# Optimization experiments

Hardware: AMD Instinct MI355X
Metric: run time of the kernel (lower is better)

The kernel has to match this reference:

```python
import jax, jax.numpy as jnp
import numpy as np

N_GRAPH = 10000
IN_DIM = 256
HID = 256
N_NODES = 16
FEAT_DIM = 64
N_EDGES = 5
TAU = 0.01


def _gat(x, src, dst, W, al, ar, R, b, H, D, N):
    # DGL GATConv: fc -> per-head attention logits -> edge softmax over dst -> aggregate, residual fc, bias
    h = (x @ W).reshape(N, H, D)                      # [N,H,D]
    el = jnp.sum(h * al[None], -1)                    # [N,H]
    er = jnp.sum(h * ar[None], -1)                    # [N,H]
    e = jax.nn.leaky_relu(el[src] + er[dst], 0.2)     # [E,H]
    m = jax.ops.segment_max(e, dst, num_segments=N)
    ex = jnp.exp(e - m[dst])
    s = jax.ops.segment_sum(ex, dst, num_segments=N)
    alpha = ex / s[dst]                               # [E,H]
    out = jax.ops.segment_sum(alpha[:, :, None] * h[src], dst, num_segments=N)  # [N,H,D]
    out = out + (x @ R).reshape(N, H, D) + b.reshape(1, H, D)
    return out.reshape(N, H * D)


def _masked_softmax(vec, mask, eps=1e-8):
    m = mask.astype(vec.dtype)
    _vec = vec * m - 10000.0 * (1.0 - m)
    vmax = jnp.max(_vec, axis=-1, keepdims=True)
    exps = jnp.exp((vec - vmax) * m) * m
    return exps / (jnp.sum(exps, -1, keepdims=True) + eps)


def _sample_edges(probs, target_idx):
    n, T = probs.shape
    mask = jnp.arange(T) == target_idx                # [T] bool, one-hot of target
    edges = [jnp.full((n,), target_idx, dtype=jnp.int32)]
    key = jax.random.key(42)
    for i in range(N_EDGES - 1):
        p = _masked_softmax(probs, jnp.logical_not(mask))
        idx = jax.random.categorical(jax.random.fold_in(key, i),
                                     jnp.log(jnp.maximum(p, 1e-30)), axis=-1)  # [n]
        mask = jnp.logical_or(jax.nn.one_hot(idx, T, dtype=bool), mask)
        edges.append(idx.astype(jnp.int32))
    return jnp.stack(edges, axis=-1)                  # [n, N_EDGES]


def _forward(feat, W1a, al1a, ar1a, R1a, b1a, W1e, al1e, ar1e, R1e, b1e,
             W2a, al2a, ar2a, R2a, b2a, W2e, al2e, ar2e, R2e, b2e,
             Wt, bt, Wo, bo, src, dst, target_idx):
    N = feat.shape[0]
    tf = jax.nn.leaky_relu(feat[target_idx] @ Wt + bt, 0.01)            # [2*HID]
    a = _gat(feat, src, dst, W1a, al1a, ar1a, R1a, b1a, 4, HID // 4, N)  # [N,HID]
    e = _gat(feat, src, dst, W1e, al1e, ar1e, R1e, b1e, 4, HID // 4, N)  # [N,HID]
    a2 = jax.nn.leaky_relu(jnp.concatenate([a, e], -1) + tf, 0.01)       # [N,2*HID]
    e2 = jax.nn.leaky_relu(jnp.concatenate([e, a], -1) + tf, 0.01)
    a3 = _gat(a2, src, dst, W2a, al2a, ar2a, R2a, b2a, 4, N_NODES * FEAT_DIM // 4, N)  # [N, n_nodes*feat_dim]
    e3 = _gat(e2, src, dst, W2e, al2e, ar2e, R2e, b2e, 1, N_NODES, N)                  # [N, n_nodes]
    attr = a3.reshape(N, N_NODES, FEAT_DIM).mean(0)                     # [n_nodes, feat_dim]
    node_attr = jax.nn.leaky_relu(attr, 0.01) @ Wo + bo                 # [n_nodes, input_dim]
    probs = jax.nn.softmax(e3.T, axis=-1)                               # [n_nodes, N]
    return node_attr, probs


def setup_inputs() -> dict:
    key = jax.random.key(0)
    ks = jax.random.split(key, 32)
    N, IN, H = N_GRAPH, IN_DIM, 4
    E0 = 80000
    feat = jax.random.normal(ks[0], (N, IN), jnp.float32)
    loop = jnp.arange(N, dtype=jnp.int32)
    src = jnp.concatenate([jax.random.randint(ks[1], (E0,), 0, N, jnp.int32), loop])
    dst = jnp.concatenate([jax.random.randint(ks[2], (E0,), 0, N, jnp.int32), loop])

    def p(k, shape, fan):
        return jax.random.normal(k, shape, jnp.float32) * (1.0 / np.sqrt(fan))

    D1 = HID // 4
    D2a = N_NODES * FEAT_DIM // 4
    O2a = N_NODES * FEAT_DIM
    inp = dict(feat=feat, src=src, dst=dst, target_idx=7)
    # layer-1 attr / edge GATs
    inp.update(W1a=p(ks[3], (IN, HID), IN), al1a=p(ks[4], (H, D1), D1), ar1a=p(ks[5], (H, D1), D1),
               R1a=p(ks[6], (IN, HID), IN), b1a=p(ks[7], (HID,), HID))
    inp.update(W1e=p(ks[8], (IN, HID), IN), al1e=p(ks[9], (H, D1), D1), ar1e=p(ks[10], (H, D1), D1),
               R1e=p(ks[11], (IN, HID), IN), b1e=p(ks[12], (HID,), HID))
    # layer-2 attr GAT (4 heads) and edge GAT (1 head)
    inp.update(W2a=p(ks[13], (2 * HID, O2a), 2 * HID), al2a=p(ks[14], (H, D2a), D2a), ar2a=p(ks[15], (H, D2a), D2a),
               R2a=p(ks[16], (2 * HID, O2a), 2 * HID), b2a=p(ks[17], (O2a,), O2a))
    inp.update(W2e=p(ks[18], (2 * HID, N_NODES), 2 * HID), al2e=p(ks[19], (1, N_NODES), N_NODES),
               ar2e=p(ks[20], (1, N_NODES), N_NODES), R2e=p(ks[21], (2 * HID, N_NODES), 2 * HID),
               b2e=p(ks[22], (N_NODES,), N_NODES))
    # target feat layer and attr output layer
    inp.update(Wt=p(ks[23], (IN, 2 * HID), IN), bt=p(ks[24], (2 * HID,), 2 * HID),
               Wo=p(ks[25], (FEAT_DIM, IN), FEAT_DIM), bo=p(ks[26], (IN,), IN))
    return inp


def reference(feat, W1a, al1a, ar1a, R1a, b1a, W1e, al1e, ar1e, R1e, b1e,
              W2a, al2a, ar2a, R2a, b2a, W2e, al2e, ar2e, R2e, b2e,
              Wt, bt, Wo, bo, src, dst, target_idx):
    node_attr, probs = _forward(feat, W1a, al1a, ar1a, R1a, b1a, W1e, al1e, ar1e, R1e, b1e,
                                W2a, al2a, ar2a, R2a, b2a, W2e, al2e, ar2e, R2e, b2e,
                                Wt, bt, Wo, bo, src, dst, target_idx)
    node_edges = _sample_edges(probs, target_idx)
    # (node_attr, attr_sample_weights, node_edges, normalized_edge_sample_weights)
    return node_attr, node_attr, node_edges, probs
```

## Files before the change

kernel.cpp:

```cpp
#include <hip/hip_runtime.h>
#include <hip/hip_bf16.h>

#define NGR 10000
typedef unsigned int u32;
typedef __attribute__((ext_vector_type(8))) short short8;
typedef __attribute__((ext_vector_type(4))) float f32x4;

__device__ __forceinline__ void threefry(u32 k0, u32 k1, u32 c0, u32 c1, u32& o0, u32& o1) {
    u32 ks2 = k0 ^ k1 ^ 0x1BD11BDAu;
    u32 x0 = c0 + k0, x1 = c1 + k1;
#define TF_R(r) { x0 += x1; x1 = (x1 << r) | (x1 >> (32 - r)); x1 ^= x0; }
    TF_R(13) TF_R(15) TF_R(26) TF_R(6)
    x0 += k1; x1 += ks2 + 1u;
    TF_R(17) TF_R(29) TF_R(16) TF_R(24)
    x0 += ks2; x1 += k0 + 2u;
    TF_R(13) TF_R(15) TF_R(26) TF_R(6)
    x0 += k0; x1 += k1 + 3u;
    TF_R(17) TF_R(29) TF_R(16) TF_R(24)
    x0 += k1; x1 += ks2 + 4u;
    TF_R(13) TF_R(15) TF_R(26) TF_R(6)
    x0 += ks2; x1 += k0 + 5u;
#undef TF_R
    o0 = x0; o1 = x1;
}

__global__ void k_deg(const int* __restrict__ dst, int* __restrict__ deg, int E) {
    int i = blockIdx.x * blockDim.x + threadIdx.x;
    if (i < E) atomicAdd(&deg[dst[i]], 1);
}
__global__ void k_scan(const int* __restrict__ deg, int* __restrict__ rowptr, int n) {
    __shared__ int sums[256];
    __shared__ int excl[257];
    const int T = 256;
    int t = threadIdx.x;
    int per = (n + T - 1) / T;
    int lo = t * per, hi = min(lo + per, n);
    int s = 0;
    for (int i = lo; i < hi; ++i) s += deg[i];
    sums[t] = s;
    __syncthreads();
    if (t == 0) { int run = 0; for (int i = 0; i < T; ++i) { excl[i] = run; run += sums[i]; } excl[T] = run; }
    __syncthreads();
    int run = excl[t];
    for (int i = lo; i < hi; ++i) { rowptr[i] = run; run += deg[i]; }
    if (t == 0) rowptr[n] = excl[T];
}
__global__ void k_scatter(const int* __restrict__ dst, const int* __restrict__ rowptr,
                          int* __restrict__ cursor, int* __restrict__ colidx, int E) {
    int i = blockIdx.x * blockDim.x + threadIdx.x;
    if (i >= E) return;
    int d = dst[i];
    int pos = atomicAdd(&cursor[d], 1);
    colidx[rowptr[d] + pos] = i;
}

#define TINYF 1.17549435e-38f
__global__ __launch_bounds__(256) void k_prep(
    const float* __restrict__ feat, const int* __restrict__ tptr,
    const float* __restrict__ Wt, const float* __restrict__ bt,
    const float* __restrict__ W1a, const float* __restrict__ W1e,
    const float* __restrict__ R1a, const float* __restrict__ R1e,
    const float* __restrict__ b1a, const float* __restrict__ b1e,
    const float* __restrict__ W2a, const float* __restrict__ al2a, const float* __restrict__ ar2a,
    unsigned short* __restrict__ feathi, unsigned short* __restrict__ featlo,
    unsigned short* __restrict__ WThi, unsigned short* __restrict__ WTlo,
    float* __restrict__ tf, float* __restrict__ gum, float* __restrict__ wal,
    float* __restrict__ packb, float* __restrict__ zreg)
{
    __shared__ float sh[32 * 33];
    int b = blockIdx.x, tid = threadIdx.x;
    if (b < 2500) {
        int idx = b * 256 + tid;
        float4 v = ((const float4*)feat)[idx];
        ushort4 h, l;
        __hip_bfloat16 bb; float r;
        bb = __float2bfloat16(v.x); h.x = *(unsigned short*)&bb; r = v.x - __bfloat162float(bb);
        bb = __float2bfloat16(r);   l.x = *(unsigned short*)&bb;
        bb = __float2bfloat16(v.y); h.y = *(unsigned short*)&bb; r = v.y - __bfloat162float(bb);
        bb = __float2bfloat16(r);   l.y = *(unsigned short*)&bb;
        bb = __float2bfloat16(v.z); h.z = *(unsigned short*)&bb; r = v.z - __bfloat162float(bb);
        bb = __float2bfloat16(r);   l.z = *(unsigned short*)&bb;
        bb = __float2bfloat16(v.w); h.w = *(unsigned short*)&bb; r = v.w - __bfloat162float(bb);
        bb = __float2bfloat16(r);   l.w = *(unsigned short*)&bb;
        ((ushort4*)feathi)[idx] = h;
        ((ushort4*)featlo)[idx] = l;
        return;
    }
    b -= 2500;
    if (b < 256) {
        int bx = b >> 3, by = b & 7;
        int tx = tid & 31, ty = tid >> 5;
#pragma unroll
        for (int i = ty; i < 32; i += 8) {
            int k = by * 32 + i, c = bx * 32 + tx;
            float v;
            if (c < 256) v = W1a[k * 256 + c];
            else if (c < 512) v = W1e[k * 256 + c - 256];
            else if (c < 768) v = R1a[k * 256 + c - 512];
            else v = R1e[k * 256 + c - 768];
            sh[i * 33 + tx] = v;
        }
        __syncthreads();
#pragma unroll
        for (int i = ty; i < 32; i += 8) {
            float x = sh[tx * 33 + i];
            __hip_bfloat16 bh = __float2bfloat16(x);
            float r = x - __bfloat162float(bh);
            __hip_bfloat16 bl = __float2bfloat16(r);
            WThi[(size_t)(bx * 32 + i) * 256 + by * 32 + tx] = *(unsigned short*)&bh;
            WTlo[(size_t)(bx * 32 + i) * 256 + by * 32 + tx] = *(unsigned short*)&bl;
        }
        return;
    }
    b -= 256;
    if (b < 8) {
        float* frow = sh;
        float* red = sh + 256;
        int t = *tptr;
        frow[tid] = feat[t * 256 + tid];
        __syncthreads();
        int j = b * 64 + (tid & 63);
        int ks = (tid >> 6) * 64;
        float s = 0.f;
#pragma unroll 16
        for (int k = ks; k < ks + 64; ++k) s = fmaf(frow[k], Wt[(size_t)k * 512 + j], s);
        red[tid] = s;
        __syncthreads();
        if (tid < 64) {
            float v = red[tid] + red[tid + 64] + red[tid + 128] + red[tid + 192] + bt[j];
            tf[j] = v >= 0.f ? v : 0.01f * v;
        }
        return;
    }
    b -= 8;
    if (b < 2500) {
        int idx = b * 256 + tid;
        int it = idx / (16 * NGR);
        int f = idx - it * (16 * NGR);
        u32 fk0, fk1, o0, o1;
        threefry(0u, 42u, 0u, (u32)it, fk0, fk1);
        threefry(fk0, fk1, 0u, (u32)f, o0, o1);
        u32 bits = o0 ^ o1;
        float fl = __uint_as_float((bits >> 9) | 0x3F800000u) - 1.0f;
        float u = fmaxf(TINYF, fl + TINYF);
        gum[idx] = -logf(-logf(u));
        return;
    }
    b -= 2500;
    if (b < 16) {
        int o = b * 256 + tid;
        int k = o >> 3, q = o & 7, sel = q >> 2, hh = q & 3;
        const float* av = (sel ? ar2a : al2a) + hh * 256;
        const float* wr = W2a + (size_t)k * 1024 + hh * 256;
        float s = 0.f;
        for (int d = 0; d < 256; ++d) s = fmaf(wr[d], av[d], s);
        wal[k * 8 + q] = s;
        return;
    }
    b -= 16;
    if (b < 235) {
        int idx = b * 256 + tid;
        if (idx < NGR * 6) zreg[idx] = 0.f;
        return;
    }
    b -= 235;
    {
        int c = b * 256 + tid;
        packb[c] = (c < 512) ? 0.f : ((c < 768) ? b1a[c - 512] : b1e[c - 768]);
    }
}

__global__ __launch_bounds__(256) void gemm_bf16x3(
    const unsigned short* __restrict__ Ahi, const unsigned short* __restrict__ Alo,
    const unsigned short* __restrict__ Bhi, const unsigned short* __restrict__ Blo,
    float* __restrict__ C, const float* __restrict__ bias, int M)
{
    constexpr int K = 256;
    __shared__ unsigned short AsH[2][128 * 32];
    __shared__ unsigned short AsL[2][128 * 32];
    __shared__ unsigned short BsH[2][128 * 32];
    __shared__ unsigned short BsL[2][128 * 32];
    const int tid = threadIdx.x;
    const int lane = tid & 63;
    const int w = tid >> 6, wr = w >> 1, wc = w & 1;
    const int bm = blockIdx.y * 128, bn = blockIdx.x * 128;
    const int fr = lane & 15, fq = lane >> 4;
    const int srow = tid >> 2;
    const int sbyte = (tid & 3) * 16;
    f32x4 acc[4][4] = {};

    auto stage = [&](int b, int k0) {
        const char* pA[2] = {(const char*)Ahi, (const char*)Alo};
        const char* pB[2] = {(const char*)Bhi, (const char*)Blo};
        char* dA[2] = {(char*)AsH[b], (char*)AsL[b]};
        char* dB[2] = {(char*)BsH[b], (char*)BsL[b]};
#pragma unroll
        for (int q = 0; q < 2; ++q) {
            const char* ga0 = pA[q] + ((size_t)(bm + srow) * K + k0) * 2 + sbyte;
            const char* ga1 = pA[q] + ((size_t)(bm + 64 + srow) * K + k0) * 2 + sbyte;
            const char* gb0 = pB[q] + ((size_t)(bn + srow) * K + k0) * 2 + sbyte;
            const char* gb1 = pB[q] + ((size_t)(bn + 64 + srow) * K + k0) * 2 + sbyte;
            __builtin_amdgcn_global_load_lds((const __attribute__((address_space(1))) void*)ga0,
                (__attribute__((address_space(3))) void*)(dA[q] + tid * 16), 16, 0, 0);
            __builtin_amdgcn_global_load_lds((const __attribute__((address_space(1))) void*)ga1,
                (__attribute__((address_space(3))) void*)(dA[q] + 4096 + tid * 16), 16, 0, 0);
            __builtin_amdgcn_global_load_lds((const __attribute__((address_space(1))) void*)gb0,
                (__attribute__((address_space(3))) void*)(dB[q] + tid * 16), 16, 0, 0);
            __builtin_amdgcn_global_load_lds((const __attribute__((address_space(1))) void*)gb1,
                (__attribute__((address_space(3))) void*)(dB[q] + 4096 + tid * 16), 16, 0, 0);
        }
    };

    stage(0, 0);
    __syncthreads();
    int buf = 0;
    for (int t = 0; t < 8; ++t) {
        if (t < 7) stage(buf ^ 1, (t + 1) * 32);
        const char* ah = (const char*)AsH[buf];
        const char* al = (const char*)AsL[buf];
        const char* bh = (const char*)BsH[buf];
        const char* bl = (const char*)BsL[buf];
        short8 afh[4], afl[4], bfh[4], bfl[4];
#pragma unroll
        for (int m = 0; m < 4; ++m) {
            int o = (wr * 64 + m * 16 + fr) * 64 + fq * 16;
            afh[m] = *(const short8*)(ah + o);
            afl[m] = *(const short8*)(al + o);
        }
#pragma unroll
        for (int n = 0; n < 4; ++n) {
            int o = (wc * 64 + n * 16 + fr) * 64 + fq * 16;
            bfh[n] = *(const short8*)(bh + o);
            bfl[n] = *(const short8*)(bl + o);
        }
#pragma unroll
        for (int m = 0; m < 4; ++m)
#pragma unroll
            for (int n = 0; n < 4; ++n) {
                acc[m][n] = __builtin_amdgcn_mfma_f32_16x16x32_bf16(afl[m], bfh[n], acc[m][n], 0, 0, 0);
                acc[m][n] = __builtin_amdgcn_mfma_f32_16x16x32_bf16(afh[m], bfl[n], acc[m][n], 0, 0, 0);
                acc[m][n] = __builtin_amdgcn_mfma_f32_16x16x32_bf16(afh[m], bfh[n], acc[m][n], 0, 0, 0);
            }
        __syncthreads();
        buf ^= 1;
    }
#pragma unroll
    for (int m = 0; m < 4; ++m) {
#pragma unroll
        for (int i = 0; i < 4; ++i) {
            int row = bm + wr * 64 + m * 16 + fq * 4 + i;
            if (row >= M) continue;
#pragma unroll
            for (int n = 0; n < 4; ++n) {
                int col = bn + wc * 64 + n * 16 + fr;
                C[(size_t)row * 1024 + col] = acc[m][n][i] + bias[col];
            }
        }
    }
}

__global__ void k_el_er_l1(const float* __restrict__ h,
                           const float* __restrict__ al1a, const float* __restrict__ ar1a,
                           const float* __restrict__ al1e, const float* __restrict__ ar1e,
                           float* __restrict__ el, float* __restrict__ er, int N)
{
    int idx = blockIdx.x * blockDim.x + threadIdx.x;
    if (idx >= N * 8) return;
    int n = idx >> 3, sub = idx & 7;
    int role = sub >> 2, hh = sub & 3;
    const float* hp = h + (size_t)n * 1024 + role * 256 + hh * 64;
    const float* alp = (role ? al1e : al1a) + hh * 64;
    const float* arp = (role ? ar1e : ar1a) + hh * 64;
    float sl = 0.f, sr = 0.f;
    for (int d = 0; d < 64; d += 4) {
        float4 v = *(const float4*)(hp + d);
        float4 a4 = *(const float4*)(alp + d);
        float4 r4 = *(const float4*)(arp + d);
        sl = fmaf(v.x, a4.x, sl); sl = fmaf(v.y, a4.y, sl); sl = fmaf(v.z, a4.z, sl); sl = fmaf(v.w, a4.w, sl);
        sr = fmaf(v.x, r4.x, sr); sr = fmaf(v.y, r4.y, sr); sr = fmaf(v.z, r4.z, sr); sr = fmaf(v.w, r4.w, sr);
    }
    el[n * 8 + sub] = sl;
    er[n * 8 + sub] = sr;
}

__global__ void k_softmax_csr(const float* __restrict__ el, const float* __restrict__ er,
                              const int* __restrict__ rowptr, const int* __restrict__ colidx,
                              const int* __restrict__ src,
                              float* __restrict__ ee, int H, int hshift, int total)
{
    int idx = blockIdx.x * blockDim.x + threadIdx.x;
    if (idx >= total) return;
    int n = idx >> hshift, hh = idx & (H - 1);
    float ern = er[n * H + hh];
    int i0 = rowptr[n], i1 = rowptr[n + 1];
    float mx = -INFINITY;
    for (int i = i0; i < i1; ++i) {
        float v = el[src[colidx[i]] * H + hh] + ern;
        v = v >= 0.f ? v : 0.2f * v;
        mx = fmaxf(mx, v);
    }
    float s = 0.f;
    for (int i = i0; i < i1; ++i) {
        int e = colidx[i];
        float v = el[src[e] * H + hh] + ern;
        v = v >= 0.f ? v : 0.2f * v;
        float ex = expf(v - mx);
        ee[(size_t)e * H + hh] = ex;
        s += ex;
    }
    for (int i = i0; i < i1; ++i) {
        int e = colidx[i];
        ee[(size_t)e * H + hh] /= s;
    }
}

__global__ void k_agg_acc(const float* __restrict__ alpha,
                          const int* __restrict__ rowptr, const int* __restrict__ colidx,
                          const int* __restrict__ src,
                          const float* __restrict__ regionA,
                          float* __restrict__ accb, int total)
{
    int idx = blockIdx.x * blockDim.x + threadIdx.x;
    if (idx >= total) return;
    int n = idx >> 7, c4 = idx & 127;
    int hh = c4 >> 4;
    const float4* h4 = (const float4*)regionA;
    float4 acc = h4[(size_t)n * 256 + 128 + c4];
    int i = rowptr[n], i1 = rowptr[n + 1];
    for (; i + 1 < i1; i += 2) {
        int e0 = colidx[i], e1 = colidx[i + 1];
        int s0 = src[e0], s1 = src[e1];
        float a0 = alpha[(size_t)e0 * 8 + hh];
        float a1 = alpha[(size_t)e1 * 8 + hh];
        float4 h0 = h4[(size_t)s0 * 256 + c4];
        float4 h1 = h4[(size_t)s1 * 256 + c4];
        acc.x = fmaf(a0, h0.x, acc.x); acc.y = fmaf(a0, h0.y, acc.y);
        acc.z = fmaf(a0, h0.z, acc.z); acc.w = fmaf(a0, h0.w, acc.w);
        acc.x = fmaf(a1, h1.x, acc.x); acc.y = fmaf(a1, h1.y, acc.y);
        acc.z = fmaf(a1, h1.z, acc.z); acc.w = fmaf(a1, h1.w, acc.w);
    }
    if (i < i1) {
        int e0 = colidx[i];
        float a0 = alpha[(size_t)e0 * 8 + hh];
        float4 h0 = h4[(size_t)src[e0] * 256 + c4];
        acc.x = fmaf(a0, h0.x, acc.x); acc.y = fmaf(a0, h0.y, acc.y);
        acc.z = fmaf(a0, h0.z, acc.z); acc.w = fmaf(a0, h0.w, acc.w);
    }
    ((float4*)accb)[(size_t)n * 128 + c4] = acc;
}

__global__ __launch_bounds__(256) void k_node_linear(
    const float* __restrict__ accb, const float* __restrict__ tf,
    const float* __restrict__ We, const float* __restrict__ Re, const float* __restrict__ be,
    const float* __restrict__ wal,
    const float* __restrict__ al2e, const float* __restrict__ ar2e,
    float* __restrict__ h2e, float* __restrict__ e3,
    float* __restrict__ el2e, float* __restrict__ er2e,
    float* __restrict__ el2a, float* __restrict__ er2a)
{
    __shared__ float As[8 * 1024];
    __shared__ float red[2048];
    __shared__ float hl[8][16];
    int tid = threadIdx.x;
    int m0 = blockIdx.x * 8;
    for (int i = tid; i < 8 * 128; i += 256) {
        int row = i >> 7, c = (i & 127) << 2;
        float4 a = *(const float4*)(accb + (size_t)(m0 + row) * 512 + c);
        int cc = (c + 256) & 511;
        float4 ta = *(const float4*)(tf + c);
        float4 te = *(const float4*)(tf + cc);
        float4 xa, xe;
        xa.x = a.x + ta.x; xa.y = a.y + ta.y; xa.z = a.z + ta.z; xa.w = a.w + ta.w;
        xe.x = a.x + te.x; xe.y = a.y + te.y; xe.z = a.z + te.z; xe.w = a.w + te.w;
        xa.x = xa.x >= 0.f ? xa.x : 0.01f * xa.x;
        xa.y = xa.y >= 0.f ? xa.y : 0.01f * xa.y;
        xa.z = xa.z >= 0.f ? xa.z : 0.01f * xa.z;
        xa.w = xa.w >= 0.f ? xa.w : 0.01f * xa.w;
        xe.x = xe.x >= 0.f ? xe.x : 0.01f * xe.x;
        xe.y = xe.y >= 0.f ? xe.y : 0.01f * xe.y;
        xe.z = xe.z >= 0.f ? xe.z : 0.01f * xe.z;
        xe.w = xe.w >= 0.f ? xe.w : 0.01f * xe.w;
        *(float4*)(As + row * 1024 + c) = xa;
        *(float4*)(As + row * 1024 + 512 + cc) = xe;
    }
    __syncthreads();
    {
        int j = tid & 31, ks = tid >> 5;
        const float* B = (j < 16) ? We : Re;
        int jj = j & 15;
        float acc[8] = {};
        int k0 = ks * 64;
        for (int kk = 0; kk < 64; kk += 4) {
            int k = k0 + kk;
            float b0 = B[(k + 0) * 16 + jj];
            float b1 = B[(k + 1) * 16 + jj];
            float b2 = B[(k + 2) * 16 + jj];
            float b3 = B[(k + 3) * 16 + jj];
#pragma unroll
            for (int r = 0; r < 8; ++r) {
                float4 a = *(const float4*)(As + r * 1024 + 512 + k);
                acc[r] = fmaf(a.x, b0, acc[r]);
                acc[r] = fmaf(a.y, b1, acc[r]);
                acc[r] = fmaf(a.z, b2, acc[r]);
                acc[r] = fmaf(a.w, b3, acc[r]);
            }
        }
#pragma unroll
        for (int r = 0; r < 8; ++r) red[(r * 32 + j) * 8 + ks] = acc[r];
    }
    __syncthreads();
    {
        int r = tid >> 5, jo = tid & 31;
        const float* rp = red + (r * 32 + jo) * 8;
        float acc = ((rp[0] + rp[1]) + (rp[2] + rp[3])) + ((rp[4] + rp[5]) + (rp[6] + rp[7]));
        int m = m0 + r, jj = jo & 15;
        if (jo < 16) { h2e[(size_t)m * 16 + jj] = acc; hl[r][jj] = acc; }
        else         e3[(size_t)m * 16 + jj] = acc + be[jj];
    }
    __syncthreads();
    {
        int q = tid & 7, ks2 = tid >> 3;
        float acc[8] = {};
        int k0 = ks2 * 16;
        for (int kk = 0; kk < 16; ++kk) {
            int k = k0 + kk;
            float b = wal[k * 8 + q];
#pragma unroll
            for (int r = 0; r < 8; ++r)
                acc[r] = fmaf(As[r * 1024 + k], b, acc[r]);
        }
#pragma unroll
        for (int r = 0; r < 8; ++r) red[(r * 8 + q) * 32 + ks2] = acc[r];
    }
    __syncthreads();
    if (tid < 64) {
        const float* rp = red + tid * 32;
        float acc = 0.f;
#pragma unroll
        for (int g = 0; g < 32; ++g) acc += rp[g];
        int r = tid >> 3, q = tid & 7;
        int m = m0 + r;
        if (q < 4) el2a[m * 4 + q] = acc;
        else       er2a[m * 4 + (q - 4)] = acc;
    }
    if (tid >= 64 && tid < 72) {
        int rr = tid - 64;
        float sl = 0.f, sr = 0.f;
        const float* hp = hl[rr];
        for (int d = 0; d < 16; ++d) { float v = hp[d]; sl = fmaf(v, al2e[d], sl); sr = fmaf(v, ar2e[d], sr); }
        el2e[m0 + rr] = sl;
        er2e[m0 + rr] = sr;
    }
}

__global__ void k_sm_l2(const float* __restrict__ el2a, const float* __restrict__ er2a,
                        const float* __restrict__ el2e, const float* __restrict__ er2e,
                        const int* __restrict__ rowptr, const int* __restrict__ colidx,
                        const int* __restrict__ src,
                        const float* __restrict__ h2e,
                        float* __restrict__ walpha, float* __restrict__ e3, int N)
{
    int idx = blockIdx.x * blockDim.x + threadIdx.x;
    if (idx < N * 4) {
        int n = idx >> 2, hh = idx & 3;
        float ern = er2a[n * 4 + hh];
        int i0 = rowptr[n], i1 = rowptr[n + 1];
        float mx = -INFINITY;
        for (int i = i0; i < i1; ++i) {
            float v = el2a[src[colidx[i]] * 4 + hh] + ern;
            v = v >= 0.f ? v : 0.2f * v;
            mx = fmaxf(mx, v);
        }
        float s = 0.f;
        for (int i = i0; i < i1; ++i) {
            float v = el2a[src[colidx[i]] * 4 + hh] + ern;
            v = v >= 0.f ? v : 0.2f * v;
            s += expf(v - mx);
        }
        for (int i = i0; i < i1; ++i) {
            int e = colidx[i];
            int sn = src[e];
            float v = el2a[sn * 4 + hh] + ern;
            v = v >= 0.f ? v : 0.2f * v;
            float alpha = expf(v - mx) / s;
            atomicAdd(&walpha[sn * 4 + hh], alpha);
        }
        return;
    }
    int n = idx - N * 4;
    if (n >= N) return;
    float ern = er2e[n];
    int i0 = rowptr[n], i1 = rowptr[n + 1];
    float mx = -INFINITY;
    for (int i = i0; i < i1; ++i) {
        float v = el2e[src[colidx[i]]] + ern;
        v = v >= 0.f ? v : 0.2f * v;
        mx = fmaxf(mx, v);
    }
    float s = 0.f;
    for (int i = i0; i < i1; ++i) {
        float v = el2e[src[colidx[i]]] + ern;
        v = v >= 0.f ? v : 0.2f * v;
        s += expf(v - mx);
    }
    float4* e34 = (float4*)(e3 + (size_t)n * 16);
    float4 a0 = e34[0], a1 = e34[1], a2 = e34[2], a3 = e34[3];
    for (int i = i0; i < i1; ++i) {
        int e = colidx[i];
        int sn = src[e];
        float v = el2e[sn] + ern;
        v = v >= 0.f ? v : 0.2f * v;
        float al = expf(v - mx) / s;
        const float4* hp = (const float4*)(h2e + (size_t)sn * 16);
        float4 h0 = hp[0], h1 = hp[1], h2 = hp[2], h3 = hp[3];
        a0.x = fmaf(al, h0.x, a0.x); a0.y = fmaf(al, h0.y, a0.y); a0.z = fmaf(al, h0.z, a0.z); a0.w = fmaf(al, h0.w, a0.w);
        a1.x = fmaf(al, h1.x, a1.x); a1.y = fmaf(al, h1.y, a1.y); a1.z = fmaf(al, h1.z, a1.z); a1.w = fmaf(al, h1.w, a1.w);
        a2.x = fmaf(al, h2.x, a2.x); a2.y = fmaf(al, h2.y, a2.y); a2.z = fmaf(al, h2.z, a2.z); a2.w = fmaf(al, h2.w, a2.w);
        a3.x = fmaf(al, h3.x, a3.x); a3.y = fmaf(al, h3.y, a3.y); a3.z = fmaf(al, h3.z, a3.z); a3.w = fmaf(al, h3.w, a3.w);
    }
    e34[0] = a0; e34[1] = a1; e34[2] = a2; e34[3] = a3;
}

__global__ __launch_bounds__(256) void k_pwa(const float* __restrict__ accb,
                                             const float* __restrict__ tf,
                                             const float* __restrict__ walpha,
                                             float* __restrict__ pwa)
{
    int b = blockIdx.x, t = threadIdx.x;
    float tf0 = tf[t], tf1 = tf[t + 256];
    float acc[5][2] = {};
    int n0 = b * 80, n1 = min(n0 + 80, NGR);
    for (int n = n0; n < n1; ++n) {
        const float* row = accb + (size_t)n * 512;
        const float* wa = walpha + n * 4;
        float w0 = wa[0], w1 = wa[1], w2 = wa[2], w3 = wa[3];
        float x0 = row[t] + tf0;       x0 = x0 >= 0.f ? x0 : 0.01f * x0;
        float x1 = row[t + 256] + tf1; x1 = x1 >= 0.f ? x1 : 0.01f * x1;
        acc[0][0] = fmaf(w0, x0, acc[0][0]); acc[0][1] = fmaf(w0, x1, acc[0][1]);
        acc[1][0] = fmaf(w1, x0, acc[1][0]); acc[1][1] = fmaf(w1, x1, acc[1][1]);
        acc[2][0] = fmaf(w2, x0, acc[2][0]); acc[2][1] = fmaf(w2, x1, acc[2][1]);
        acc[3][0] = fmaf(w3, x0, acc[3][0]); acc[3][1] = fmaf(w3, x1, acc[3][1]);
        acc[4][0] += x0; acc[4][1] += x1;
    }
#pragma unroll
    for (int q = 0; q < 5; ++q) {
        pwa[(size_t)b * 2560 + q * 512 + t] = acc[q][0];
        pwa[(size_t)b * 2560 + q * 512 + t + 256] = acc[q][1];
    }
}
__global__ void k_pwa_fin(const float* __restrict__ pwa, float* __restrict__ waw)
{
    int idx = blockIdx.x * blockDim.x + threadIdx.x;
    if (idx >= 2560) return;
    float s = 0.f;
    for (int b = 0; b < 125; ++b) s += pwa[(size_t)b * 2560 + idx];
    waw[idx] = s;
}

__global__ __launch_bounds__(256) void k_gemv3(const float* __restrict__ waw,
                                               const float* __restrict__ W2a, const float* __restrict__ R2a,
                                               const float* __restrict__ b2a,
                                               float* __restrict__ attrL)
{
    __shared__ float red[256];
    int b = blockIdx.x, t = threadIdx.x;
    int c = b * 16 + (t & 15);
    int hh = (b * 16) >> 8;
    int ks = (t >> 4) * 32;
    const float* wh = waw + hh * 512;
    const float* w4 = waw + 4 * 512;
    float s = 0.f;
#pragma unroll 8
    for (int k = ks; k < ks + 32; ++k) {
        s = fmaf(wh[k], W2a[(size_t)k * 1024 + c], s);
        s = fmaf(w4[k], R2a[(size_t)k * 1024 + c], s);
    }
    red[t] = s;
    __syncthreads();
    if (t < 16) {
        float v = 0.f;
#pragma unroll
        for (int g = 0; g < 16; ++g) v += red[t + g * 16];
        v = v / (float)NGR + b2a[b * 16 + t];
        attrL[b * 16 + t] = v >= 0.f ? v : 0.01f * v;
    }
}

__global__ __launch_bounds__(256) void k_nattr2(const float* __restrict__ attrL,
                                                const float* __restrict__ Wo, const float* __restrict__ bo,
                                                float* __restrict__ out)
{
    __shared__ float al[64];
    int i = blockIdx.x, t = threadIdx.x;
    if (t < 64) al[t] = attrL[i * 64 + t];
    __syncthreads();
    float acc = 0.f;
#pragma unroll 8
    for (int d = 0; d < 64; ++d) acc = fmaf(al[d], Wo[d * 256 + t], acc);
    acc += bo[t];
    out[i * 256 + t] = acc;
    out[4096 + i * 256 + t] = acc;
}

__global__ __launch_bounds__(256) void k_e3stats(const float* __restrict__ e3,
                                                 float* __restrict__ pm, float* __restrict__ ps)
{
    __shared__ float lds[4000];
    __shared__ float redm[16][16];
    __shared__ float reds[16][16];
    __shared__ float cm[16];
    int b = blockIdx.x, tid = threadIdx.x;
    int base = b * 250 * 16;
    for (int i = tid; i < 4000; i += 256) lds[i] = e3[base + i];
    __syncthreads();
    int c = tid & 15, g = tid >> 4;
    float mx = -INFINITY;
    for (int q = g; q < 250; q += 16) mx = fmaxf(mx, lds[q * 16 + c]);
    redm[c][g] = mx;
    __syncthreads();
    if (tid < 16) {
        float m = redm[tid][0];
        for (int q = 1; q < 16; ++q) m = fmaxf(m, redm[tid][q]);
        cm[tid] = m;
    }
    __syncthreads();
    float mb = cm[c];
    float s = 0.f;
    for (int q = g; q < 250; q += 16) s += expf(lds[q * 16 + c] - mb);
    reds[c][g] = s;
    __syncthreads();
    if (tid < 16) {
        float ss = 0.f;
        for (int q = 0; q < 16; ++q) ss += reds[tid][q];
        pm[b * 16 + tid] = cm[tid];
        ps[b * 16 + tid] = ss;
    }
}

__global__ __launch_bounds__(256) void k_top5(const float* __restrict__ e3, const float* __restrict__ gum,
                                              const float* __restrict__ pm, const float* __restrict__ ps,
                                              float* __restrict__ probs,
                                              float* __restrict__ t5v, int* __restrict__ t5i)
{
    __shared__ float wv[4];
    __shared__ int wi[4];
    int chunk = blockIdx.x, y = blockIdx.y;
    int it = y >> 4, r = y & 15;
    int tid = threadIdx.x, lane = tid & 63, wid = tid >> 6;
    float M = -INFINITY;
    for (int b = 0; b < 40; ++b) M = fmaxf(M, pm[b * 16 + r]);
    float S = 0.f;
    for (int b = 0; b < 40; ++b) S += ps[b * 16 + r] * expf(pm[b * 16 + r] - M);
    float mxr = M, ssr = S;
    const float* g = gum + (size_t)y * NGR;
    int jb = chunk * 1250;
    float sv[5]; int si[5];
#pragma unroll
    for (int q = 0; q < 5; ++q) {
        int o = q * 256 + tid;
        float s = -INFINITY; int idx = 0x7FFFFFFF;
        if (o < 1250) {
            int j = jb + o;
            float p = expf(e3[(size_t)j * 16 + r] - mxr) / ssr;
            if (it == 0) probs[(size_t)r * NGR + j] = p;
            s = g[j] + p;
            idx = j;
        }
        sv[q] = s; si[q] = idx;
    }
    int outb = (y * 8 + chunk) * 5;
    for (int round = 0; round < 5; ++round) {
        float best = sv[0]; int bi = si[0];
#pragma unroll
        for (int q = 1; q < 5; ++q)
            if (sv[q] > best || (sv[q] == best && si[q] < bi)) { best = sv[q]; bi = si[q]; }
#pragma unroll
        for (int o = 32; o > 0; o >>= 1) {
            float ov = __shfl_xor(best, o, 64); int oi = __shfl_xor(bi, o, 64);
            if (ov > best || (ov == best && oi < bi)) { best = ov; bi = oi; }
        }
        if (lane == 0) { wv[wid] = best; wi[wid] = bi; }
        __syncthreads();
        float gbv = wv[0]; int gbi = wi[0];
#pragma unroll
        for (int w2 = 1; w2 < 4; ++w2) {
            float ov = wv[w2]; int oi = wi[w2];
            if (ov > gbv || (ov == gbv && oi < gbi)) { gbv = ov; gbi = oi; }
        }
        if (tid == 0) { t5v[outb + round] = gbv; t5i[outb + round] = gbi; }
#pragma unroll
        for (int q = 0; q < 5; ++q) if (si[q] == gbi) { sv[q] = -INFINITY; si[q] = 0x7FFFFFFF; }
        __syncthreads();
    }
}

__global__ void k_select(const int* __restrict__ tptr, const float* __restrict__ t5v,
                         const int* __restrict__ t5i, float* __restrict__ out_edges)
{
    int r = threadIdx.x;
    if (r >= 16) return;
    int s0 = *tptr, s1 = -1, s2 = -1, s3 = -1;
    out_edges[r * 5] = (float)s0;
    for (int it = 0; it < 4; ++it) {
        float best = -INFINITY; int bi = 0x7FFFFFFF;
        int base = (it * 16 + r) * 40;
        for (int c = 0; c < 40; ++c) {
            int idx = t5i[base + c];
            if (idx == s0 || idx == s1 || idx == s2 || idx == s3) continue;
            float v = t5v[base + c];
            if (v > best || (v == best && idx < bi)) { best = v; bi = idx; }
        }
        if (it == 0) s1 = bi; else if (it == 1) s2 = bi; else if (it == 2) s3 = bi;
        out_edges[r * 5 + it + 1] = (float)bi;
    }
}

extern "C" void kernel_launch(void* const* d_in, const int* in_sizes, int n_in,
                              void* d_out, int out_size, void* d_ws, size_t ws_size,
                              hipStream_t stream)
{
    const float* feat = (const float*)d_in[0];
    const int* src = (const int*)d_in[1];
    const int* dst = (const int*)d_in[2];
    const int* tptr = (const int*)d_in[3];
    const float* W1a = (const float*)d_in[4];  const float* al1a = (const float*)d_in[5];
    const float* ar1a = (const float*)d_in[6]; const float* R1a = (const float*)d_in[7];
    const float* b1a = (const float*)d_in[8];
    const float* W1e = (const float*)d_in[9];  const float* al1e = (const float*)d_in[10];
    const float* ar1e = (const float*)d_in[11]; const float* R1e = (const float*)d_in[12];
    const float* b1e = (const float*)d_in[13];
    const float* W2a = (const float*)d_in[14]; const float* al2a = (const float*)d_in[15];
    const float* ar2a = (const float*)d_in[16]; const float* R2a = (const float*)d_in[17];
    const float* b2a = (const float*)d_in[18];
    const float* W2e = (const float*)d_in[19]; const float* al2e = (const float*)d_in[20];
    const float* ar2e = (const float*)d_in[21]; const float* R2e = (const float*)d_in[22];
    const float* b2e = (const float*)d_in[23];
    const float* Wt = (const float*)d_in[24];  const float* bt = (const float*)d_in[25];
    const float* Wo = (const float*)d_in[26];  const float* bo = (const float*)d_in[27];
    const int E = in_sizes[1];
    const int N = NGR;

    float* ws = (float*)d_ws;
    float* regionA = ws;
    size_t off = (size_t)N * 1024;
    auto alloc = [&](size_t n) { float* p = ws + off; off += (n + 3) & ~(size_t)3; return p; };
    float* accb = alloc((size_t)N * 512);
    float* tf   = alloc(512);
    float* el1  = alloc((size_t)N * 8);
    float* er1  = alloc((size_t)N * 8);
    float* el2a = alloc((size_t)N * 4);
    float* er2a = alloc((size_t)N * 4);
    float* el2e = alloc(N);
    float* er2e = alloc(N);
    float* h2e  = alloc((size_t)N * 16);
    float* e3   = alloc((size_t)N * 16);
    float* ee1  = alloc((size_t)E * 8);
    float* packb = alloc(1024);
    float* gum   = alloc((size_t)4 * 16 * NGR);
    float* wal   = alloc(512 * 8);
    float* pwa   = alloc(125 * 2560);
    float* waw   = alloc(2560);
    float* attrL = alloc(1024);
    float* pm    = alloc(40 * 16);
    float* ps    = alloc(40 * 16);
    float* t5v   = alloc(64 * 40);
    int*   t5i   = (int*)alloc(64 * 40);
    unsigned short* feathi = (unsigned short*)alloc((size_t)10112 * 128);
    unsigned short* featlo = (unsigned short*)alloc((size_t)10112 * 128);
    unsigned short* WThi = (unsigned short*)alloc((size_t)1024 * 128);
    unsigned short* WTlo = (unsigned short*)alloc((size_t)1024 * 128);
    float* zstart = alloc((size_t)N * 6);
    float* walpha = zstart;
    int* deg    = (int*)(zstart + (size_t)N * 4);
    int* cursor = deg + N;
    int* rowptr = (int*)alloc(N + 1);
    int* colidx = (int*)alloc(E);

    float* out = (float*)d_out;
    float* out_edges = out + 8192;
    float* out_probs = out + 8272;

    dim3 blk(256);

    k_prep<<<5519, blk, 0, stream>>>(feat, tptr, Wt, bt, W1a, W1e, R1a, R1e, b1a, b1e,
                                     W2a, al2a, ar2a, feathi, featlo, WThi, WTlo,
                                     tf, gum, wal, packb, zstart);
    k_deg<<<(E + 255) / 256, blk, 0, stream>>>(dst, deg, E);
    k_scan<<<1, blk, 0, stream>>>(deg, rowptr, N);
    k_scatter<<<(E + 255) / 256, blk, 0, stream>>>(dst, rowptr, cursor, colidx, E);

    gemm_bf16x3<<<dim3(8, 79), blk, 0, stream>>>(feathi, featlo, WThi, WTlo, regionA, packb, N);
    k_el_er_l1<<<(N * 8 + 255) / 256, blk, 0, stream>>>(regionA, al1a, ar1a, al1e, ar1e, el1, er1, N);
    k_softmax_csr<<<(N * 8 + 255) / 256, blk, 0, stream>>>(el1, er1, rowptr, colidx, src, ee1, 8, 3, N * 8);
    k_agg_acc<<<(N * 128 + 255) / 256, blk, 0, stream>>>(ee1, rowptr, colidx, src,
                                                         regionA, accb, N * 128);

    k_node_linear<<<N / 8, blk, 0, stream>>>(accb, tf, W2e, R2e, b2e, wal, al2e, ar2e,
                                             h2e, e3, el2e, er2e, el2a, er2a);
    k_sm_l2<<<(N * 5 + 255) / 256, blk, 0, stream>>>(el2a, er2a, el2e, er2e,
                                                     rowptr, colidx, src, h2e, walpha, e3, N);

    k_pwa<<<125, blk, 0, stream>>>(accb, tf, walpha, pwa);
    k_pwa_fin<<<10, blk, 0, stream>>>(pwa, waw);
    k_gemv3<<<64, blk, 0, stream>>>(waw, W2a, R2a, b2a, attrL);
    k_nattr2<<<16, blk, 0, stream>>>(attrL, Wo, bo, out);

    k_e3stats<<<40, blk, 0, stream>>>(e3, pm, ps);
    k_top5<<<dim3(8, 64), blk, 0, stream>>>(e3, gum, pm, ps, out_probs, t5v, t5i);
    k_select<<<1, 64, 0, stream>>>(tptr, t5v, t5i, out_edges);
}
```

Baseline: 314.2 us.

## Split wal dot products across threads, swizzle GEMM block order, unroll aggregation by four

Three unrelated changes. The wal precompute in k_prep now splits each 256-long dot product across 8 threads and reduces them through shared memory, using 128 blocks instead of 16 to shorten that serial tail. The bf16x3 GEMM remaps block indices so consecutive blocks walk down M within a fixed N column, aiming for better L2 reuse of B. The CSR aggregation loop is unrolled from 2 to 4 edges to keep more gather loads in flight, at the cost of more registers.

```diff
diff --git a/kernel.cpp b/kernel.cpp
--- a/kernel.cpp
+++ b/kernel.cpp
@@ -147,17 +147,25 @@
         return;
     }
     b -= 2500;
-    if (b < 16) {
+    if (b < 128) {
         int o = b * 256 + tid;
-        int k = o >> 3, q = o & 7, sel = q >> 2, hh = q & 3;
-        const float* av = (sel ? ar2a : al2a) + hh * 256;
-        const float* wr = W2a + (size_t)k * 1024 + hh * 256;
+        int outi = o >> 3, sl = o & 7;
+        int k = outi >> 3, q = outi & 7, sel = q >> 2, hh = q & 3;
+        const float* av = (sel ? ar2a : al2a) + hh * 256 + sl * 32;
+        const float* wr = W2a + (size_t)k * 1024 + hh * 256 + sl * 32;
         float s = 0.f;
-        for (int d = 0; d < 256; ++d) s = fmaf(wr[d], av[d], s);
-        wal[k * 8 + q] = s;
+#pragma unroll 8
+        for (int d = 0; d < 32; ++d) s = fmaf(wr[d], av[d], s);
+        sh[tid] = s;
+        __syncthreads();
+        if ((tid & 7) == 0) {
+            float v = ((sh[tid] + sh[tid + 1]) + (sh[tid + 2] + sh[tid + 3])) +
+                      ((sh[tid + 4] + sh[tid + 5]) + (sh[tid + 6] + sh[tid + 7]));
+            wal[outi] = v;
+        }
         return;
     }
-    b -= 16;
+    b -= 128;
     if (b < 235) {
         int idx = b * 256 + tid;
         if (idx < NGR * 6) zreg[idx] = 0.f;
@@ -183,7 +191,9 @@
     const int tid = threadIdx.x;
     const int lane = tid & 63;
     const int w = tid >> 6, wr = w >> 1, wc = w & 1;
-    const int bm = blockIdx.y * 128, bn = blockIdx.x * 128;
+    int lin = blockIdx.y * 8 + blockIdx.x;
+    int wg = (lin & 7) * 79 + (lin >> 3);
+    const int bm = (wg >> 3) * 128, bn = (wg & 7) * 128;
     const int fr = lane & 15, fq = lane >> 4;
     const int srow = tid >> 2;
     const int sbyte = (tid & 3) * 16;
@@ -327,19 +337,27 @@
     const float4* h4 = (const float4*)regionA;
     float4 acc = h4[(size_t)n * 256 + 128 + c4];
     int i = rowptr[n], i1 = rowptr[n + 1];
-    for (; i + 1 < i1; i += 2) {
-        int e0 = colidx[i], e1 = colidx[i + 1];
-        int s0 = src[e0], s1 = src[e1];
+    for (; i + 3 < i1; i += 4) {
+        int e0 = colidx[i], e1 = colidx[i + 1], e2 = colidx[i + 2], e3 = colidx[i + 3];
+        int s0 = src[e0], s1 = src[e1], s2 = src[e2], s3 = src[e3];
         float a0 = alpha[(size_t)e0 * 8 + hh];
         float a1 = alpha[(size_t)e1 * 8 + hh];
+        float a2 = alpha[(size_t)e2 * 8 + hh];
+        float a3 = alpha[(size_t)e3 * 8 + hh];
         float4 h0 = h4[(size_t)s0 * 256 + c4];
         float4 h1 = h4[(size_t)s1 * 256 + c4];
+        float4 h2 = h4[(size_t)s2 * 256 + c4];
+        float4 h3 = h4[(size_t)s3 * 256 + c4];
         acc.x = fmaf(a0, h0.x, acc.x); acc.y = fmaf(a0, h0.y, acc.y);
         acc.z = fmaf(a0, h0.z, acc.z); acc.w = fmaf(a0, h0.w, acc.w);
         acc.x = fmaf(a1, h1.x, acc.x); acc.y = fmaf(a1, h1.y, acc.y);
         acc.z = fmaf(a1, h1.z, acc.z); acc.w = fmaf(a1, h1.w, acc.w);
-    }
-    if (i < i1) {
+        acc.x = fmaf(a2, h2.x, acc.x); acc.y = fmaf(a2, h2.y, acc.y);
+        acc.z = fmaf(a2, h2.z, acc.z); acc.w = fmaf(a2, h2.w, acc.w);
+        acc.x = fmaf(a3, h3.x, acc.x); acc.y = fmaf(a3, h3.y, acc.y);
+        acc.z = fmaf(a3, h3.z, acc.z); acc.w = fmaf(a3, h3.w, acc.w);
+    }
+    for (; i < i1; ++i) {
         int e0 = colidx[i];
         float a0 = alpha[(size_t)e0 * 8 + hh];
         float4 h0 = h4[(size_t)src[e0] * 256 + c4];
@@ -782,7 +800,7 @@
 
     dim3 blk(256);
 
-    k_prep<<<5519, blk, 0, stream>>>(feat, tptr, Wt, bt, W1a, W1e, R1a, R1e, b1a, b1e,
+    k_prep<<<5631, blk, 0, stream>>>(feat, tptr, Wt, bt, W1a, W1e, R1a, R1e, b1a, b1e,
                                      W2a, al2a, ar2a, feathi, featlo, WThi, WTlo,
                                      tf, gum, wal, packb, zstart);
     k_deg<<<(E + 255) / 256, blk, 0, stream>>>(dst, deg, E);
```

Result: faster. 300.4 us (-4.4%).
